# Performance work log

Hardware: AMD Instinct MI355X
Metric: run time of the kernel (lower is better)

## Reference

```python
import jax, jax.numpy as jnp
import numpy as np

STRIDE = 4.0      # fpn_strides[0]
POOL = 7          # roi_align_size
SR = 2            # roi_align_sampling_ratio
NUM_CLASSES = 10
B, N = 2, 512
C, H, W = 256, 256, 256
OUT = 1024


def _bilinear(feat_hwc, y, x):
    # feat_hwc: [H, W, C]; y, x: [N, 7, 7, SR, SR] sample coords (feature units)
    Hf, Wf, _ = feat_hwc.shape
    valid = (y > -1.0) & (y < Hf) & (x > -1.0) & (x < Wf)
    y = jnp.clip(y, 0.0, Hf - 1.0)
    x = jnp.clip(x, 0.0, Wf - 1.0)
    y0 = jnp.floor(y)
    x0 = jnp.floor(x)
    y0i = y0.astype(jnp.int32)
    x0i = x0.astype(jnp.int32)
    y1i = jnp.minimum(y0i + 1, Hf - 1)
    x1i = jnp.minimum(x0i + 1, Wf - 1)
    ly = (y - y0)[..., None]
    lx = (x - x0)[..., None]
    hy = 1.0 - ly
    hx = 1.0 - lx
    v = (hy * hx * feat_hwc[y0i, x0i] + hy * lx * feat_hwc[y0i, x1i]
         + ly * hx * feat_hwc[y1i, x0i] + ly * lx * feat_hwc[y1i, x1i])
    return v * valid[..., None]


def _roi_align_rotated(feat_hwc, boxes):
    # boxes: [N, 5] = (cx, cy, w, h, theta) in feature coords -> [N, 7, 7, C]
    cx, cy, w, h, th = (boxes[:, k] for k in range(5))
    bins = jnp.arange(POOL, dtype=feat_hwc.dtype)
    sub = (jnp.arange(SR, dtype=feat_hwc.dtype) + 0.5) / SR
    # local (box-frame) coords of sample points along each axis: [N, 7, SR]
    ys = -h[:, None, None] / 2 + (h / POOL)[:, None, None] * (bins[None, :, None] + sub[None, None, :])
    xs = -w[:, None, None] / 2 + (w / POOL)[:, None, None] * (bins[None, :, None] + sub[None, None, :])
    yy = ys[:, :, None, :, None]  # [N,7,1,SR,1]
    xx = xs[:, None, :, None, :]  # [N,1,7,1,SR]
    cos = jnp.cos(th)[:, None, None, None, None]
    sin = jnp.sin(th)[:, None, None, None, None]
    gx = cx[:, None, None, None, None] + xx * cos - yy * sin
    gy = cy[:, None, None, None, None] + xx * sin + yy * cos
    v = _bilinear(feat_hwc, gy, gx)  # [N,7,7,SR,SR,C]
    return v.mean(axis=(3, 4))       # average-pool the SRxSR samples per bin


def norm_angle(a):
    return (a + jnp.pi / 2) % jnp.pi - jnp.pi / 2


def setup_inputs():
    key = jax.random.key(0)
    ks = jax.random.split(key, 14)
    feat = jax.random.normal(ks[0], (B, C, H, W), jnp.float32)
    cx = jax.random.uniform(ks[1], (B, N), minval=16.0, maxval=H - 16.0)
    cy = jax.random.uniform(ks[2], (B, N), minval=16.0, maxval=W - 16.0)
    bw = jax.random.uniform(ks[3], (B, N), minval=8.0, maxval=64.0)
    bh = jax.random.uniform(ks[4], (B, N), minval=8.0, maxval=64.0)
    th = jax.random.uniform(ks[5], (B, N), minval=-np.pi / 2, maxval=np.pi / 2)
    proposals = jnp.stack([cx, cy, bw, bh, th], axis=-1).astype(jnp.float32)
    d_in = C * POOL * POOL
    s = 0.02
    return {
        'feat': feat,
        'proposals': proposals,
        'W1': jax.random.normal(ks[6], (d_in, OUT), jnp.float32) * s,
        'b1': jnp.zeros((OUT,), jnp.float32),
        'W2': jax.random.normal(ks[7], (OUT, OUT), jnp.float32) * s,
        'b2': jnp.zeros((OUT,), jnp.float32),
        'Wcls': jax.random.normal(ks[8], (OUT, NUM_CLASSES + 1), jnp.float32) * s,
        'bcls': jnp.zeros((NUM_CLASSES + 1,), jnp.float32),
        'Wreg': jax.random.normal(ks[9], (OUT, 5), jnp.float32) * s,
        'breg': jnp.zeros((5,), jnp.float32),
    }


def reference(feat, proposals, W1, b1, W2, b2, Wcls, bcls, Wreg, breg):
    Bn, Nn = proposals.shape[:2]
    feat_hwc = jnp.transpose(feat, (0, 2, 3, 1))  # [B,H,W,C]
    pooled = jax.vmap(_roi_align_rotated)(feat_hwc, proposals)  # [B,N,7,7,C]
    # torch flattens [N, C, 7, 7] -> C*49; match that layout
    x = jnp.transpose(pooled, (0, 1, 4, 2, 3)).reshape(Bn, Nn, -1)
    x = jax.nn.relu(x @ W1 + b1)
    x = jax.nn.relu(x @ W2 + b2)
    cls = x @ Wcls + bcls   # [B,N,11]
    reg = x @ Wreg + breg   # [B,N,5]
    # decode (proposals scaled to image coords by stride; theta unscaled)
    scale = jnp.array([STRIDE, STRIDE, STRIDE, STRIDE, 1.0], feat.dtype)
    p = proposals * scale
    clamp_v = float(abs(np.log(16.0 / 1000.0)))
    bx = p[..., 2] * reg[..., 0] + p[..., 0]
    by = p[..., 3] * reg[..., 1] + p[..., 1]
    bw = p[..., 2] * jnp.exp(jnp.clip(reg[..., 2], -clamp_v, clamp_v))
    bh = p[..., 3] * jnp.exp(jnp.clip(reg[..., 3], -clamp_v, clamp_v))
    ba = norm_angle(p[..., 4] + reg[..., 4])
    boxes = jnp.stack([bx, by, bw, bh, ba], axis=-1)
    return boxes, cls
```

## Files before the change

kernel.cpp:

```cpp
#include <hip/hip_runtime.h>
#include <math.h>
#include <stdint.h>

#define BB 2
#define NN 512
#define CC 256
#define HH 256
#define WW 256
#define DIN 12544
#define OUT1 1024
#define NCLS 11
#define NROI 1024
#define SK1 8
#define SK2 2
#define NWB 1696

typedef short bf16x8 __attribute__((ext_vector_type(8)));
typedef float f32x4 __attribute__((ext_vector_type(4)));
typedef unsigned short u16x8 __attribute__((ext_vector_type(8)));

__device__ inline unsigned short f2bf(float f) {
  unsigned int u = __float_as_uint(f);
  u += 0x7FFF + ((u >> 16) & 1);
  return (unsigned short)(u >> 16);
}
__device__ inline float bf2f(unsigned short h) {
  return __uint_as_float(((unsigned int)h) << 16);
}

__device__ inline void gll16(const void* g, void* l) {
  __builtin_amdgcn_global_load_lds(
      reinterpret_cast<const __attribute__((address_space(1))) void*>(
          reinterpret_cast<uintptr_t>(g)),
      reinterpret_cast<__attribute__((address_space(3))) void*>(
          (unsigned int)reinterpret_cast<uintptr_t>(l)),
      16, 0, 0);
}

__global__ __launch_bounds__(256) void prep_feat(
    const float* __restrict__ feat, unsigned short* __restrict__ fhwc) {
  __shared__ unsigned short tile[64 * 132];
  int bid = blockIdx.x;
  int tid = threadIdx.x;
  int hw0 = (bid & 511) * 128;
  int c0 = ((bid >> 9) & 3) * 64;
  int b = bid >> 11;
  int cl_base = tid >> 5;
  int hwq = (tid & 31) * 4;
#pragma unroll
  for (int pass = 0; pass < 8; ++pass) {
    int cl = cl_base + pass * 8;
    float4 v = *(const float4*)(feat + ((size_t)b * CC + c0 + cl) * (HH * WW) +
                                hw0 + hwq);
    ushort4 o;
    o.x = f2bf(v.x); o.y = f2bf(v.y); o.z = f2bf(v.z); o.w = f2bf(v.w);
    *(ushort4*)&tile[cl * 132 + hwq] = o;
  }
  __syncthreads();
  int hi = tid >> 4, lo = tid & 15;
#pragma unroll
  for (int pass = 0; pass < 8; ++pass) {
    int hwl = hi + pass * 16;
    int cq = lo * 4;
    ushort4 o;
    o.x = tile[(cq + 0) * 132 + hwl];
    o.y = tile[(cq + 1) * 132 + hwl];
    o.z = tile[(cq + 2) * 132 + hwl];
    o.w = tile[(cq + 3) * 132 + hwl];
    *(ushort4*)(fhwc + ((size_t)b * (HH * WW) + hw0 + hwl) * CC + c0 + cq) = o;
  }
}

__device__ inline void bilin(float gy, float gx, int& y0, int& x0, int& y1,
                             int& x1, float& w00, float& w01, float& w10,
                             float& w11) {
  float valid = (gy > -1.f && gy < 256.f && gx > -1.f && gx < 256.f) ? 0.25f : 0.f;
  float y = fminf(fmaxf(gy, 0.f), 255.f);
  float x = fminf(fmaxf(gx, 0.f), 255.f);
  float yf = floorf(y), xf = floorf(x);
  y0 = (int)yf; x0 = (int)xf;
  y1 = min(y0 + 1, 255); x1 = min(x0 + 1, 255);
  float ly = y - yf, lx = x - xf, hy = 1.f - ly, hx = 1.f - lx;
  w00 = hy * hx * valid; w01 = hy * lx * valid;
  w10 = ly * hx * valid; w11 = ly * lx * valid;
}

__global__ __launch_bounds__(256) void roi_fused(
    const unsigned short* __restrict__ fhwc, const float* __restrict__ props,
    unsigned short* __restrict__ pooled, const float* __restrict__ W1,
    unsigned short* __restrict__ W1T, const float* __restrict__ W2,
    unsigned short* __restrict__ W2T, int roi_cnt) {
  __shared__ unsigned short tile[64 * 132];
  int bid = blockIdx.x;
  int tid = threadIdx.x;

  if (bid >= roi_cnt) {
    int u = bid - roi_cnt;
    const float* in;
    unsigned short* out;
    int Kout, kblk, nblk;
    bool perm;
    if (u < 1568) {
      in = W1; out = W1T; Kout = DIN; kblk = u % 196; nblk = u / 196;
      perm = true;
    } else {
      u -= 1568;
      in = W2; out = W2T; Kout = OUT1; kblk = u & 15; nblk = u >> 4;
      perm = false;
    }
    int k0 = kblk * 64, n0 = nblk * 128;
    int kl_base = tid >> 5;
    int nq = (tid & 31) * 4;
#pragma unroll
    for (int pass = 0; pass < 8; ++pass) {
      int kl = kl_base + pass * 8;
      int k = k0 + kl;
      int row = perm ? ((k & 255) * 49 + (k >> 8)) : k;
      float4 v = *(const float4*)(in + (size_t)row * OUT1 + n0 + nq);
      ushort4 o;
      o.x = f2bf(v.x); o.y = f2bf(v.y); o.z = f2bf(v.z); o.w = f2bf(v.w);
      *(ushort4*)&tile[kl * 132 + nq] = o;
    }
    __syncthreads();
    int hi = tid >> 4, lo = tid & 15;
#pragma unroll
    for (int pass = 0; pass < 8; ++pass) {
      int nl = hi + pass * 16;
      int kq = lo * 4;
      ushort4 o;
      o.x = tile[(kq + 0) * 132 + nl];
      o.y = tile[(kq + 1) * 132 + nl];
      o.z = tile[(kq + 2) * 132 + nl];
      o.w = tile[(kq + 3) * 132 + nl];
      *(ushort4*)(out + (size_t)(n0 + nl) * Kout + k0 + kq) = o;
    }
    return;
  }

  int roi = bid >> 1;
  int half = bid & 1;
  int b = roi >> 9;
  const float* p = props + (size_t)roi * 5;
  float cx = p[0], cy = p[1], w = p[2], h = p[3], th = p[4];
  float sn = sinf(th), cs = cosf(th);
  int wave = tid >> 6, lane = tid & 63;
  int hi32 = lane >> 5;
  int c8 = (lane & 31) * 8;
  const unsigned short* fb = fhwc + (size_t)b * HH * WW * CC;
  unsigned short* outp = pooled + (size_t)roi * DIN;

  for (int bin = half * 4 + wave; bin < 49; bin += 8) {
    int py = bin / 7, px = bin - py * 7;
    float acc[8] = {0.f, 0.f, 0.f, 0.f, 0.f, 0.f, 0.f, 0.f};
    const unsigned short* ptr[8];
    float wsel[8];
#pragma unroll
    for (int s = 0; s < 4; ++s) {
      int sy = s >> 1, sx = s & 1;
      float ys = -0.5f * h + (h / 7.0f) * ((float)py + ((float)sy + 0.5f) * 0.5f);
      float xs = -0.5f * w + (w / 7.0f) * ((float)px + ((float)sx + 0.5f) * 0.5f);
      float gx = cx + xs * cs - ys * sn;
      float gy = cy + xs * sn + ys * cs;
      int y0, x0, y1, x1; float w00, w01, w10, w11;
      bilin(gy, gx, y0, x0, y1, x1, w00, w01, w10, w11);
      int xa = hi32 ? x1 : x0;
      ptr[s * 2 + 0] = fb + ((size_t)(y0 * WW + xa)) * CC + c8;
      wsel[s * 2 + 0] = hi32 ? w01 : w00;
      ptr[s * 2 + 1] = fb + ((size_t)(y1 * WW + xa)) * CC + c8;
      wsel[s * 2 + 1] = hi32 ? w11 : w10;
    }
    u16x8 v[8];
#pragma unroll
    for (int t = 0; t < 8; ++t) v[t] = *(const u16x8*)ptr[t];
#pragma unroll
    for (int t = 0; t < 8; ++t) {
      float wt = wsel[t];
#pragma unroll
      for (int e = 0; e < 8; ++e) acc[e] += wt * bf2f(v[t][e]);
    }
#pragma unroll
    for (int e = 0; e < 8; ++e) acc[e] += __shfl_xor(acc[e], 32);
    if (lane < 32) {
      u16x8 o;
#pragma unroll
      for (int e = 0; e < 8; ++e) o[e] = f2bf(acc[e]);
      *(u16x8*)(outp + bin * 256 + c8) = o;
    }
  }
}

__global__ __launch_bounds__(256) void roi_align_nchw(
    const float* __restrict__ feat, const float* __restrict__ props,
    unsigned short* __restrict__ pooled) {
  int roi = blockIdx.x;
  int b = roi >> 9;
  int c = threadIdx.x;
  const float* p = props + (size_t)roi * 5;
  float cx = p[0], cy = p[1], w = p[2], h = p[3], th = p[4];
  float sn = sinf(th), cs = cosf(th);
  const float* fb = feat + ((size_t)b * CC + c) * (HH * WW);
  unsigned short* outp = pooled + (size_t)roi * DIN;
  for (int bin = 0; bin < 49; ++bin) {
    int py = bin / 7, px = bin - py * 7;
    float acc = 0.f;
#pragma unroll
    for (int sy = 0; sy < 2; ++sy) {
#pragma unroll
      for (int sx = 0; sx < 2; ++sx) {
        float ys = -0.5f * h + (h / 7.0f) * ((float)py + ((float)sy + 0.5f) * 0.5f);
        float xs = -0.5f * w + (w / 7.0f) * ((float)px + ((float)sx + 0.5f) * 0.5f);
        float gx = cx + xs * cs - ys * sn;
        float gy = cy + xs * sn + ys * cs;
        int y0, x0, y1, x1; float w00, w01, w10, w11;
        bilin(gy, gx, y0, x0, y1, x1, w00, w01, w10, w11);
        acc += w00 * fb[(size_t)y0 * WW + x0] + w01 * fb[(size_t)y0 * WW + x1] +
               w10 * fb[(size_t)y1 * WW + x0] + w11 * fb[(size_t)y1 * WW + x1];
      }
    }
    outp[bin * 256 + c] = f2bf(acc);
  }
}

__global__ __launch_bounds__(256) void gemm_mfma_128(
    const unsigned short* __restrict__ A, const unsigned short* __restrict__ Bw,
    float* __restrict__ part, int K, int Ks) {
  __shared__ short As[128 * 32];
  __shared__ short Bs[128 * 32];
  int tid = threadIdx.x;
  int w = tid >> 6, lane = tid & 63;
  int quad = lane >> 4, l16 = lane & 15;
  int m0 = blockIdx.y * 128, n0 = blockIdx.x * 128;
  int bz = blockIdx.z;
  int wm = w >> 1, wn = w & 1;

  const char* pA = (const char*)A +
      ((size_t)(m0 + 32 * w + (lane >> 2)) * K + (size_t)bz * Ks) * 2 +
      (lane & 3) * 16;
  const char* pB = (const char*)Bw +
      ((size_t)(n0 + 32 * w + (lane >> 2)) * K + (size_t)bz * Ks) * 2 +
      (lane & 3) * 16;
  short* la = &As[w * 1024];
  short* lb = &Bs[w * 1024];
  const size_t rstep = (size_t)K * 2 * 16;

  f32x4 acc[4][4] = {};
  int aoff[4], boff[4];
#pragma unroll
  for (int t = 0; t < 4; ++t) {
    aoff[t] = (wm * 64 + t * 16 + l16) * 32 + quad * 8;
    boff[t] = (wn * 64 + t * 16 + l16) * 32 + quad * 8;
  }

  for (int kk = 0; kk < Ks; kk += 32) {
    __syncthreads();
    gll16(pA, la);
    gll16(pA + rstep, la + 512);
    gll16(pB, lb);
    gll16(pB + rstep, lb + 512);
    pA += 64; pB += 64;
    __syncthreads();
    bf16x8 af[4], bfr[4];
#pragma unroll
    for (int t = 0; t < 4; ++t) af[t] = *(const bf16x8*)&As[aoff[t]];
#pragma unroll
    for (int t = 0; t < 4; ++t) bfr[t] = *(const bf16x8*)&Bs[boff[t]];
#pragma unroll
    for (int mt = 0; mt < 4; ++mt)
#pragma unroll
      for (int nt = 0; nt < 4; ++nt)
        acc[mt][nt] = __builtin_amdgcn_mfma_f32_16x16x32_bf16(
            af[mt], bfr[nt], acc[mt][nt], 0, 0, 0);
  }

  float* pp = part + (size_t)bz * (OUT1 * NROI);
#pragma unroll
  for (int mt = 0; mt < 4; ++mt)
#pragma unroll
    for (int nt = 0; nt < 4; ++nt) {
      int col = n0 + wn * 64 + nt * 16 + l16;
#pragma unroll
      for (int r = 0; r < 4; ++r) {
        int row = m0 + wm * 64 + mt * 16 + quad * 4 + r;
        pp[(size_t)row * OUT1 + col] = acc[mt][nt][r];
      }
    }
}

__global__ __launch_bounds__(256) void reduce_relu_bf16(
    const float* __restrict__ part, const float* __restrict__ bias,
    unsigned short* __restrict__ out) {
  int i = blockIdx.x * 256 + threadIdx.x;
  int base = i * 4;
  int col = base & (OUT1 - 1);
  const float4* p = (const float4*)part;
  float4 s = p[i];
#pragma unroll
  for (int z = 1; z < SK1; ++z) {
    float4 t = p[i + (size_t)z * (NROI * OUT1 / 4)];
    s.x += t.x; s.y += t.y; s.z += t.z; s.w += t.w;
  }
  float4 bv = *(const float4*)(bias + col);
  ushort4 o;
  o.x = f2bf(fmaxf(s.x + bv.x, 0.f));
  o.y = f2bf(fmaxf(s.y + bv.y, 0.f));
  o.z = f2bf(fmaxf(s.z + bv.z, 0.f));
  o.w = f2bf(fmaxf(s.w + bv.w, 0.f));
  *(ushort4*)(out + base) = o;
}

__global__ __launch_bounds__(256) void gemm_mfma_64_part(
    const unsigned short* __restrict__ A, const unsigned short* __restrict__ Bw,
    float* __restrict__ part, int K, int Ks) {
  __shared__ short As[64 * 64];
  __shared__ short Bs[64 * 64];
  int tid = threadIdx.x;
  int w = tid >> 6, lane = tid & 63;
  int quad = lane >> 4, l16 = lane & 15;
  int m0 = blockIdx.y * 64, n0 = blockIdx.x * 64;
  int bz = blockIdx.z;
  int wm = w >> 1, wn = w & 1;

  const char* pA = (const char*)A +
      ((size_t)(m0 + 16 * w + (lane >> 3)) * K + (size_t)bz * Ks) * 2 +
      (lane & 7) * 16;
  const char* pB = (const char*)Bw +
      ((size_t)(n0 + 16 * w + (lane >> 3)) * K + (size_t)bz * Ks) * 2 +
      (lane & 7) * 16;
  short* la = &As[w * 1024];
  short* lb = &Bs[w * 1024];
  const size_t rstep = (size_t)K * 2 * 8;

  f32x4 acc[2][2] = {};
  int aoff[2], boff[2];
#pragma unroll
  for (int t = 0; t < 2; ++t) {
    aoff[t] = (wm * 32 + t * 16 + l16) * 64 + quad * 8;
    boff[t] = (wn * 32 + t * 16 + l16) * 64 + quad * 8;
  }

  for (int kk = 0; kk < Ks; kk += 64) {
    __syncthreads();
    gll16(pA, la);
    gll16(pA + rstep, la + 512);
    gll16(pB, lb);
    gll16(pB + rstep, lb + 512);
    pA += 128; pB += 128;
    __syncthreads();
#pragma unroll
    for (int ks = 0; ks < 2; ++ks) {
      bf16x8 af[2], bfr[2];
#pragma unroll
      for (int t = 0; t < 2; ++t) af[t] = *(const bf16x8*)&As[aoff[t] + ks * 32];
#pragma unroll
      for (int t = 0; t < 2; ++t) bfr[t] = *(const bf16x8*)&Bs[boff[t] + ks * 32];
#pragma unroll
      for (int mt = 0; mt < 2; ++mt)
#pragma unroll
        for (int nt = 0; nt < 2; ++nt)
          acc[mt][nt] = __builtin_amdgcn_mfma_f32_16x16x32_bf16(
              af[mt], bfr[nt], acc[mt][nt], 0, 0, 0);
    }
  }
  float* pp = part + (size_t)bz * (OUT1 * NROI);
#pragma unroll
  for (int mt = 0; mt < 2; ++mt)
#pragma unroll
    for (int nt = 0; nt < 2; ++nt) {
      int col = n0 + wn * 32 + nt * 16 + l16;
#pragma unroll
      for (int r = 0; r < 4; ++r) {
        int row = m0 + wm * 32 + mt * 16 + quad * 4 + r;
        pp[(size_t)row * OUT1 + col] = acc[mt][nt][r];
      }
    }
}

__global__ __launch_bounds__(256) void head_kernel(
    const float* __restrict__ P0, const float* __restrict__ P1,
    const float* __restrict__ b2, const float* __restrict__ Wcls,
    const float* __restrict__ bcls, const float* __restrict__ Wreg,
    const float* __restrict__ breg, const float* __restrict__ props,
    float* __restrict__ out) {
  __shared__ float xrow[1024];
  __shared__ float partial[16][17];
  __shared__ float res[16];
  int row = blockIdx.x;
  int tid = threadIdx.x;
  {
    size_t off = (size_t)row * 1024 + tid * 4;
    float4 a = *(const float4*)(P0 + off);
    float4 b = *(const float4*)(P1 + off);
    float4 bv = *(const float4*)(b2 + tid * 4);
    xrow[tid * 4 + 0] = fmaxf(a.x + b.x + bv.x, 0.f);
    xrow[tid * 4 + 1] = fmaxf(a.y + b.y + bv.y, 0.f);
    xrow[tid * 4 + 2] = fmaxf(a.z + b.z + bv.z, 0.f);
    xrow[tid * 4 + 3] = fmaxf(a.w + b.w + bv.w, 0.f);
  }
  __syncthreads();
  int col = tid & 15, slice = tid >> 4;
  float s = 0.f;
  if (col < NCLS) {
    for (int k = slice * 64; k < slice * 64 + 64; ++k)
      s += xrow[k] * Wcls[(size_t)k * NCLS + col];
  } else {
    int rc = col - NCLS;
    for (int k = slice * 64; k < slice * 64 + 64; ++k)
      s += xrow[k] * Wreg[(size_t)k * 5 + rc];
  }
  partial[slice][col] = s;
  __syncthreads();
  if (tid < 16) {
    float t = 0.f;
    for (int sl = 0; sl < 16; ++sl) t += partial[sl][tid];
    t += (tid < NCLS) ? bcls[tid] : breg[tid - NCLS];
    res[tid] = t;
  }
  __syncthreads();
  if (tid < NCLS) out[5120 + (size_t)row * NCLS + tid] = res[tid];
  if (tid == 0) {
    const float* p = props + (size_t)row * 5;
    float p0 = p[0] * 4.f, p1 = p[1] * 4.f, p2 = p[2] * 4.f, p3 = p[3] * 4.f,
          p4 = p[4];
    float r0 = res[11], r1 = res[12], r2 = res[13], r3 = res[14], r4 = res[15];
    const float V = 4.135166556742356f;
    float bx = p2 * r0 + p0;
    float by = p3 * r1 + p1;
    float bw = p2 * expf(fminf(fmaxf(r2, -V), V));
    float bh = p3 * expf(fminf(fmaxf(r3, -V), V));
    const float PI = 3.14159265358979323846f;
    float a = p4 + r4;
    float m = fmodf(a + PI * 0.5f, PI);
    if (m < 0.f) m += PI;
    float ba = m - PI * 0.5f;
    float* bo = out + (size_t)row * 5;
    bo[0] = bx; bo[1] = by; bo[2] = bw; bo[3] = bh; bo[4] = ba;
  }
}

extern "C" void kernel_launch(void* const* d_in, const int* in_sizes, int n_in,
                              void* d_out, int out_size, void* d_ws,
                              size_t ws_size, hipStream_t stream) {
  const float* feat  = (const float*)d_in[0];
  const float* props = (const float*)d_in[1];
  const float* W1    = (const float*)d_in[2];
  const float* b1    = (const float*)d_in[3];
  const float* W2    = (const float*)d_in[4];
  const float* b2    = (const float*)d_in[5];
  const float* Wcls  = (const float*)d_in[6];
  const float* bcls  = (const float*)d_in[7];
  const float* Wreg  = (const float*)d_in[8];
  const float* breg  = (const float*)d_in[9];
  float* out = (float*)d_out;

  char* wp = (char*)d_ws;
  unsigned short* pooled = (unsigned short*)wp; wp += (size_t)NROI * DIN * 2;
  unsigned short* W1T    = (unsigned short*)wp; wp += (size_t)OUT1 * DIN * 2;
  unsigned short* W2T    = (unsigned short*)wp; wp += (size_t)OUT1 * OUT1 * 2;
  unsigned short* x1     = (unsigned short*)wp; wp += (size_t)NROI * OUT1 * 2;
  float*          part1  = (float*)wp;          wp += (size_t)SK1 * NROI * OUT1 * 4;
  float*          part2  = (float*)wp;          wp += (size_t)SK2 * NROI * OUT1 * 4;
  unsigned short* fhwc   = (unsigned short*)wp;

  size_t need_min  = (size_t)(wp - (char*)d_ws);
  size_t need_full = need_min + (size_t)BB * CC * HH * WW * 2;

  if (ws_size >= need_full) {
    prep_feat<<<BB * 4 * (HH * WW / 128), 256, 0, stream>>>(feat, fhwc);
    roi_fused<<<NROI * 2 + NWB, 256, 0, stream>>>(fhwc, props, pooled, W1, W1T,
                                                  W2, W2T, NROI * 2);
  } else {
    roi_fused<<<NWB, 256, 0, stream>>>(fhwc, props, pooled, W1, W1T, W2, W2T,
                                       0);
    roi_align_nchw<<<NROI, 256, 0, stream>>>(feat, props, pooled);
  }

  gemm_mfma_128<<<dim3(8, 8, SK1), 256, 0, stream>>>(pooled, W1T, part1, DIN,
                                                     DIN / SK1);
  reduce_relu_bf16<<<NROI * OUT1 / 1024, 256, 0, stream>>>(part1, b1, x1);
  gemm_mfma_64_part<<<dim3(16, 16, SK2), 256, 0, stream>>>(x1, W2T, part2, OUT1,
                                                           OUT1 / SK2);
  head_kernel<<<NROI, 256, 0, stream>>>(part2, part2 + (size_t)NROI * OUT1, b2,
                                        Wcls, bcls, Wreg, breg, props, out);
}
```

Baseline: 378.3 us.

## Restructure NCHW-to-HWC bf16 transpose with larger tiles and fewer blocks

Rewrites the feature-map transpose kernel so each block covers 1024 spatial positions by 64 channels, handled as eight 8-channel sub-slices staged through LDS. The grid shrinks from 4096 to 512 blocks. Each thread reads contiguous float4 runs per channel and writes 16 bytes per HWC row, aiming for longer read streams and less per-block overhead. The trade-off is less parallelism, two barriers per sub-slice, and strided 16-byte writes that can reduce write coalescing.

```diff
diff --git a/kernel.cpp b/kernel.cpp
--- a/kernel.cpp
+++ b/kernel.cpp
@@ -39,35 +39,39 @@
 
 __global__ __launch_bounds__(256) void prep_feat(
     const float* __restrict__ feat, unsigned short* __restrict__ fhwc) {
-  __shared__ unsigned short tile[64 * 132];
+  __shared__ unsigned short lds[8][1032];
   int bid = blockIdx.x;
   int tid = threadIdx.x;
-  int hw0 = (bid & 511) * 128;
-  int c0 = ((bid >> 9) & 3) * 64;
-  int b = bid >> 11;
-  int cl_base = tid >> 5;
-  int hwq = (tid & 31) * 4;
-#pragma unroll
-  for (int pass = 0; pass < 8; ++pass) {
-    int cl = cl_base + pass * 8;
-    float4 v = *(const float4*)(feat + ((size_t)b * CC + c0 + cl) * (HH * WW) +
-                                hw0 + hwq);
-    ushort4 o;
-    o.x = f2bf(v.x); o.y = f2bf(v.y); o.z = f2bf(v.z); o.w = f2bf(v.w);
-    *(ushort4*)&tile[cl * 132 + hwq] = o;
-  }
-  __syncthreads();
-  int hi = tid >> 4, lo = tid & 15;
-#pragma unroll
-  for (int pass = 0; pass < 8; ++pass) {
-    int hwl = hi + pass * 16;
-    int cq = lo * 4;
-    ushort4 o;
-    o.x = tile[(cq + 0) * 132 + hwl];
-    o.y = tile[(cq + 1) * 132 + hwl];
-    o.z = tile[(cq + 2) * 132 + hwl];
-    o.w = tile[(cq + 3) * 132 + hwl];
-    *(ushort4*)(fhwc + ((size_t)b * (HH * WW) + hw0 + hwl) * CC + c0 + cq) = o;
+  int cg = bid & 3;
+  int hwt = (bid >> 2) & 63;
+  int b = bid >> 8;
+  int hw0 = hwt * 1024;
+  int c0 = cg * 64;
+  int ch = tid >> 5;
+  int j = tid & 31;
+
+  for (int sub = 0; sub < 8; ++sub) {
+    const float* src =
+        feat + ((size_t)b * CC + c0 + sub * 8 + ch) * (HH * WW) + hw0;
+#pragma unroll
+    for (int p = 0; p < 8; ++p) {
+      float4 v = *(const float4*)(src + p * 128 + j * 4);
+      ushort4 o;
+      o.x = f2bf(v.x); o.y = f2bf(v.y); o.z = f2bf(v.z); o.w = f2bf(v.w);
+      *(ushort4*)&lds[ch][p * 128 + j * 4] = o;
+    }
+    __syncthreads();
+    unsigned short* dst = fhwc + ((size_t)b * (HH * WW) + hw0) * CC + c0 + sub * 8;
+#pragma unroll
+    for (int q = 0; q < 4; ++q) {
+      int r = q * 256 + tid;
+      ushort4 lo, hi;
+      lo.x = lds[0][r]; lo.y = lds[1][r]; lo.z = lds[2][r]; lo.w = lds[3][r];
+      hi.x = lds[4][r]; hi.y = lds[5][r]; hi.z = lds[6][r]; hi.w = lds[7][r];
+      *(ushort4*)(dst + (size_t)r * CC) = lo;
+      *(ushort4*)(dst + (size_t)r * CC + 4) = hi;
+    }
+    __syncthreads();
   }
 }
 
@@ -465,7 +469,7 @@
   size_t need_full = need_min + (size_t)BB * CC * HH * WW * 2;
 
   if (ws_size >= need_full) {
-    prep_feat<<<BB * 4 * (HH * WW / 128), 256, 0, stream>>>(feat, fhwc);
+    prep_feat<<<512, 256, 0, stream>>>(feat, fhwc);
     roi_fused<<<NROI * 2 + NWB, 256, 0, stream>>>(fhwc, props, pooled, W1, W1T,
                                                   W2, W2T, NROI * 2);
   } else {
```

Measured after the change: 423.7 us. +12.0%, slower.
